# Kernel tuning notes

Hardware: AMD Instinct MI355X
Metric: run time of the kernel (lower is better)

## Reference

```python
import jax, jax.numpy as jnp
import numpy as np

D_MODEL = 1024
D_STATE = 16
D_CONV = 4
EXPAND = 2
D_INNER = D_MODEL * EXPAND
B_SZ, L_SEQ = 4, 1024


def setup_inputs() -> dict:
    key = jax.random.key(0)
    ks = jax.random.split(key, 8)
    s = lambda fan_in: 1.0 / np.sqrt(fan_in)
    x = jax.random.normal(ks[0], (B_SZ, L_SEQ, D_MODEL), dtype=jnp.float32)
    in_proj_w = jax.random.uniform(ks[1], (2 * D_INNER, D_MODEL), jnp.float32, -s(D_MODEL), s(D_MODEL))
    conv_w = jax.random.uniform(ks[2], (D_INNER, 1, D_CONV), jnp.float32, -s(D_CONV), s(D_CONV))
    conv_b = jax.random.uniform(ks[3], (D_INNER,), jnp.float32, -s(D_CONV), s(D_CONV))
    x_proj_w = jax.random.uniform(ks[4], (2 * D_STATE + D_INNER, D_INNER), jnp.float32, -s(D_INNER), s(D_INNER))
    dt_proj_w = jax.random.uniform(ks[5], (D_INNER, D_INNER), jnp.float32, -s(D_INNER), s(D_INNER))
    dt_proj_b = jax.random.uniform(ks[6], (D_INNER,), jnp.float32, -1e-3, 1e-3)
    A = jnp.tile(jnp.arange(1, D_STATE + 1, dtype=jnp.float32), (D_INNER, 1))
    A_log = jnp.log(A)
    D_param = jnp.ones((D_INNER,), jnp.float32)
    out_proj_w = jax.random.uniform(ks[7], (D_MODEL, D_INNER), jnp.float32, -s(D_INNER), s(D_INNER))
    return {"x": x, "in_proj_w": in_proj_w, "conv_w": conv_w, "conv_b": conv_b,
            "x_proj_w": x_proj_w, "dt_proj_w": dt_proj_w, "dt_proj_b": dt_proj_b,
            "A_log": A_log, "D_param": D_param, "out_proj_w": out_proj_w}


def _selective_scan(x, delta, Bp, Cp, A_log, D_param):
    # x, delta: [B, L, D]; Bp, Cp: [B, L, N]
    A = -jnp.exp(A_log)                                   # [D, N]
    deltaA = jnp.exp(delta[..., None] * A)                # [B, L, D, N]
    deltaB_x = delta[..., None] * Bp[:, :, None, :] * x[..., None]  # [B, L, D, N]

    def step(h, inp):
        dA, dBx, Ct = inp                                 # [B,D,N], [B,D,N], [B,N]
        h = dA * h + dBx
        y = jnp.einsum('bn,bdn->bd', Ct, h)
        return h, y

    h0 = jnp.zeros((x.shape[0], x.shape[2], A.shape[1]), x.dtype)
    xs = (jnp.swapaxes(deltaA, 0, 1), jnp.swapaxes(deltaB_x, 0, 1), jnp.swapaxes(Cp, 0, 1))
    _, ys = jax.lax.scan(step, h0, xs)                    # ys: [L, B, D]
    return jnp.swapaxes(ys, 0, 1) + x * D_param


def reference(x, in_proj_w, conv_w, conv_b, x_proj_w, dt_proj_w, dt_proj_b, A_log, D_param, out_proj_w):
    B, L, _ = x.shape
    xz = x @ in_proj_w.T                                  # [B, L, 2*D_inner]
    xi, z = jnp.split(xz, 2, axis=-1)
    # causal depthwise conv (pad left K-1 == pad both & truncate to L)
    xc = jnp.swapaxes(xi, 1, 2)                           # [B, D_inner, L]
    xc = jax.lax.conv_general_dilated(xc, conv_w, window_strides=(1,),
                                      padding=[(D_CONV - 1, 0)],
                                      feature_group_count=D_INNER,
                                      dimension_numbers=('NCH', 'OIH', 'NCH'))
    xc = xc + conv_b[None, :, None]
    xi = jax.nn.silu(jnp.swapaxes(xc, 1, 2))              # [B, L, D_inner]
    deltaBC = xi @ x_proj_w.T
    delta, Bp, Cp = jnp.split(deltaBC, [D_INNER, D_INNER + D_STATE], axis=-1)
    delta = jax.nn.softplus(delta @ dt_proj_w.T + dt_proj_b)
    y = _selective_scan(xi, delta, Bp, Cp, A_log, D_param)
    return (y * jax.nn.silu(z)) @ out_proj_w.T
```

## Files before the change

kernel.cpp:

```cpp
#include <hip/hip_runtime.h>
#include <math.h>

#define B_SZ 4
#define L_SEQ 1024
#define D_MODEL 1024
#define D_INNER 2048
#define D_STATE 16
#define N_BC 2080
#define M_ROWS (B_SZ * L_SEQ)
#define CHUNK 32
#define NCH (L_SEQ / CHUNK)

typedef unsigned short u16;
typedef __bf16 bf16x8 __attribute__((ext_vector_type(8)));
typedef float f32x4 __attribute__((ext_vector_type(4)));

typedef const __attribute__((address_space(1))) unsigned short glb_u16;
typedef __attribute__((address_space(3))) unsigned short lds_u16;

__device__ __forceinline__ void gload_lds16(const u16* g, u16* l) {
    __builtin_amdgcn_global_load_lds((glb_u16*)g, (lds_u16*)l, 16, 0, 0);
}

__device__ __forceinline__ float bf2f(u16 u) {
    union { unsigned int i; float f; } v; v.i = ((unsigned int)u) << 16; return v.f;
}
__device__ __forceinline__ u16 f2bf(float f) {
    union { float f; unsigned int i; } v; v.f = f;
    return (u16)((v.i + 0x7FFFu + ((v.i >> 16) & 1u)) >> 16);
}
__device__ __forceinline__ float softplus_f(float v) {
    return fmaxf(v, 0.f) + log1pf(expf(-fabsf(v)));
}
__device__ __forceinline__ float silu_f(float v) {
    return v / (1.f + expf(-v));
}

__global__ __launch_bounds__(256) void cvt5_bf16_k(
    const float* __restrict__ s0, const float* __restrict__ s1,
    const float* __restrict__ s2, const float* __restrict__ s3,
    const float* __restrict__ s4,
    u16* __restrict__ dst,
    int e0, int e1, int e2, int e3, int e4)
{
    int i = blockIdx.x * 256 + threadIdx.x;
    if (i >= e4) return;
    const float* src; int base;
    if (i < e0)      { src = s0; base = 0;  }
    else if (i < e1) { src = s1; base = e0; }
    else if (i < e2) { src = s2; base = e1; }
    else if (i < e3) { src = s3; base = e2; }
    else             { src = s4; base = e3; }
    float4 v = *(const float4*)(src + (size_t)(i - base) * 4);
    ushort4 o;
    o.x = f2bf(v.x); o.y = f2bf(v.y); o.z = f2bf(v.z); o.w = f2bf(v.w);
    *(ushort4*)(dst + (size_t)i * 4) = o;
}

__global__ __launch_bounds__(256) void transpose_cvt_k(
    const float* __restrict__ in,
    u16* __restrict__ outT)
{
    __shared__ float t[32][33];
    const int bx = blockIdx.x, by = blockIdx.y;
    const int r = threadIdx.x >> 5, c = threadIdx.x & 31;
#pragma unroll
    for (int i = 0; i < 4; ++i) {
        int kk = by * 32 + r + i * 8;
        int jj = bx * 32 + c;
        t[r + i * 8][c] = in[(size_t)kk * 2048 + jj];
    }
    __syncthreads();
#pragma unroll
    for (int i = 0; i < 4; ++i) {
        int jj = bx * 32 + r + i * 8;
        int kk = by * 32 + c;
        outT[(size_t)jj * 2048 + kk] = f2bf(t[c][r + i * 8]);
    }
}

template <int EPI, int BM, int BN, int WTM, int WTN>
__global__ __launch_bounds__((BM / WTM) * (BN / WTN) * 64, 2)
void gemm_bf16(
    const u16* __restrict__ A, int lda,
    const u16* __restrict__ W, int ldw,
    int M, int N, int K, int ldc,
    const float* __restrict__ bias,
    float* __restrict__ Cf, u16* __restrict__ Cb, float* __restrict__ Caux)
{
    constexpr int NWC = BN / WTN;
    constexpr int WAVES = (BM / WTM) * NWC;
    constexpr int MF = WTM / 16;
    constexpr int NF = WTN / 16;
    constexpr int CA = BM / 16;
    constexpr int CB = BN / 16;
    constexpr int CPW = (CA + CB) / WAVES;

    __shared__ __align__(16) u16 As[BM * 32];
    __shared__ __align__(16) u16 Ws[BN * 32];

    const unsigned nwg = gridDim.x * gridDim.y;
    const unsigned f = blockIdx.y * gridDim.x + blockIdx.x;
    const unsigned tile = (f & 7u) * (nwg >> 3) + (f >> 3);
    const int bxi = tile % gridDim.x;
    const int byi = tile / gridDim.x;

    const int tid = threadIdx.x;
    const int lane = tid & 63;
    const int wave = tid >> 6;
    const int wr = wave / NWC;
    const int wc = wave % NWC;
    const int bm = byi * BM;
    const int bn = bxi * BN;
    const int l15 = lane & 15;
    const int lq = lane >> 4;

    const int lrow = lane >> 2;
    const int qoff = (((lane & 3) ^ ((lane >> 3) & 3))) * 8;
    const int rq = ((lq ^ ((l15 >> 1) & 3))) * 8;

    f32x4 acc[MF][NF];
#pragma unroll
    for (int m = 0; m < MF; ++m)
#pragma unroll
        for (int n = 0; n < NF; ++n) acc[m][n] = f32x4{0.f, 0.f, 0.f, 0.f};

    const int nt = K >> 5;
    for (int t = 0; t < nt; ++t) {
        const int k0 = t << 5;
#pragma unroll
        for (int i = 0; i < CPW; ++i) {
            const int c = wave * CPW + i;
            if (c < CA) {
                const int row = c * 16 + lrow;
                gload_lds16(A + (size_t)(bm + row) * lda + k0 + qoff, &As[c * 512]);
            } else {
                const int cc = c - CA;
                const int row = cc * 16 + lrow;
                int wrow = bn + row; if (wrow >= N) wrow = N - 1;
                gload_lds16(W + (size_t)wrow * ldw + k0 + qoff, &Ws[cc * 512]);
            }
        }
        __syncthreads();

        bf16x8 af[MF], bfr[NF];
#pragma unroll
        for (int m = 0; m < MF; ++m) {
            int r = wr * WTM + m * 16 + l15;
            af[m] = *reinterpret_cast<const bf16x8*>(&As[r * 32 + rq]);
        }
#pragma unroll
        for (int n = 0; n < NF; ++n) {
            int r = wc * WTN + n * 16 + l15;
            bfr[n] = *reinterpret_cast<const bf16x8*>(&Ws[r * 32 + rq]);
        }
#pragma unroll
        for (int m = 0; m < MF; ++m)
#pragma unroll
            for (int n = 0; n < NF; ++n)
                acc[m][n] = __builtin_amdgcn_mfma_f32_16x16x32_bf16(af[m], bfr[n], acc[m][n], 0, 0, 0);

        __syncthreads();
    }

#pragma unroll
    for (int m = 0; m < MF; ++m) {
#pragma unroll
        for (int n = 0; n < NF; ++n) {
#pragma unroll
            for (int j = 0; j < 4; ++j) {
                int gr = bm + wr * WTM + m * 16 + lq * 4 + j;
                int gc = bn + wc * WTN + n * 16 + l15;
                float v = acc[m][n][j];
                if (EPI == 0) {
                    if (gc < N) Cf[(size_t)gr * ldc + gc] = v;
                } else if (EPI == 2) {
                    if (gc < N) Cb[(size_t)gr * ldc + gc] = f2bf(v);
                } else {
                    if (gc < D_INNER) Cf[(size_t)gr * D_INNER + gc] = softplus_f(v + bias[gc]);
                    else if (gc < N_BC) Caux[(size_t)gr * 32 + (gc - D_INNER)] = v;
                }
            }
        }
    }
}

__global__ __launch_bounds__(256) void conv_silu_k(
    const u16* __restrict__ xz,
    const float* __restrict__ cw,
    const float* __restrict__ cb,
    u16* __restrict__ xc)
{
    int idx = blockIdx.x * 256 + threadIdx.x;
    if (idx >= M_ROWS * D_INNER) return;
    int d = idx & (D_INNER - 1);
    int m = idx >> 11;
    int l = m & (L_SEQ - 1);
    float4 w = *(const float4*)(cw + d * 4);
    const u16* base = xz + (size_t)m * (2 * D_INNER) + d;
    float acc = cb[d];
    acc = fmaf(bf2f(base[0]), w.w, acc);
    if (l >= 1) acc = fmaf(bf2f(base[-(2 * D_INNER)]), w.z, acc);
    if (l >= 2) acc = fmaf(bf2f(base[-2 * (2 * D_INNER)]), w.y, acc);
    if (l >= 3) acc = fmaf(bf2f(base[-3 * (2 * D_INNER)]), w.x, acc);
    xc[idx] = f2bf(silu_f(acc));
}

__global__ __launch_bounds__(256) void scan_pass1(
    const float* __restrict__ delta,
    const u16* __restrict__ xc,
    const float* __restrict__ BC,
    const float* __restrict__ A_log,
    float* __restrict__ hbuf,
    float* __restrict__ sumd)
{
    __shared__ float Bs[CHUNK][16];
    const int bid = blockIdx.x;
    const int c = bid & (NCH - 1);
    const int dblk = (bid >> 5) & 7;
    const int b = bid >> 8;
    const int tid = threadIdx.x;
    const int d = dblk * 256 + tid;
    const int row0 = b * L_SEQ + c * CHUNK;

#pragma unroll
    for (int i = 0; i < 2; ++i) {
        int e = tid + i * 256;
        int l = e >> 4, n = e & 15;
        Bs[l][n] = BC[(size_t)(row0 + l) * 32 + n];
    }
    __syncthreads();

    float Ac[16], h[16];
#pragma unroll
    for (int n = 0; n < 16; ++n) { Ac[n] = -__expf(A_log[d * 16 + n]); h[n] = 0.f; }
    float sd = 0.f;

    for (int l = 0; l < CHUNK; ++l) {
        size_t r = (size_t)(row0 + l);
        float dv = delta[r * D_INNER + d];
        float xv = bf2f(xc[r * D_INNER + d]);
        float t = dv * xv;
        sd += dv;
#pragma unroll
        for (int n = 0; n < 16; ++n) {
            float dA = __expf(dv * Ac[n]);
            h[n] = fmaf(dA, h[n], t * Bs[l][n]);
        }
    }
    size_t base = ((size_t)(b * NCH + c) * 16) * D_INNER + d;
#pragma unroll
    for (int n = 0; n < 16; ++n) hbuf[base + (size_t)n * D_INNER] = h[n];
    sumd[(size_t)(b * NCH + c) * D_INNER + d] = sd;
}

__global__ __launch_bounds__(256) void scan_pass2(
    const float* __restrict__ A_log,
    const float* __restrict__ sumd,
    float* __restrict__ hbuf)
{
    const int bid = blockIdx.x;
    const int dblk = bid & 7;
    const int n = (bid >> 3) & 15;
    const int b = bid >> 7;
    const int d = dblk * 256 + threadIdx.x;
    const float Ac = -__expf(A_log[d * 16 + n]);
    float carry = 0.f;
    for (int c = 0; c < NCH; ++c) {
        float sd = sumd[(size_t)(b * NCH + c) * D_INNER + d];
        size_t idx = ((size_t)(b * NCH + c) * 16 + n) * D_INNER + d;
        float tmp = hbuf[idx];
        hbuf[idx] = carry;
        carry = fmaf(__expf(Ac * sd), carry, tmp);
    }
}

__global__ __launch_bounds__(256) void scan_pass3(
    const float* __restrict__ delta,
    const u16* __restrict__ xc,
    const float* __restrict__ BC,
    const u16* __restrict__ xz,
    const float* __restrict__ A_log,
    const float* __restrict__ Dp,
    const float* __restrict__ hbuf,
    u16* __restrict__ yg)
{
    __shared__ float BCs[CHUNK][32];
    const int bid = blockIdx.x;
    const int c = bid & (NCH - 1);
    const int dblk = (bid >> 5) & 7;
    const int b = bid >> 8;
    const int tid = threadIdx.x;
    const int d = dblk * 256 + tid;
    const int row0 = b * L_SEQ + c * CHUNK;

#pragma unroll
    for (int i = 0; i < (CHUNK * 32) / 256; ++i) {
        int e = tid + i * 256;
        int l = e >> 5, j = e & 31;
        BCs[l][j] = BC[(size_t)(row0 + l) * 32 + j];
    }
    __syncthreads();

    float Ac[16], h[16];
    size_t base = ((size_t)(b * NCH + c) * 16) * D_INNER + d;
#pragma unroll
    for (int n = 0; n < 16; ++n) {
        Ac[n] = -__expf(A_log[d * 16 + n]);
        h[n] = hbuf[base + (size_t)n * D_INNER];
    }
    const float Dv = Dp[d];

    for (int l = 0; l < CHUNK; ++l) {
        size_t r = (size_t)(row0 + l);
        float dv = delta[r * D_INNER + d];
        float xv = bf2f(xc[r * D_INNER + d]);
        float t = dv * xv;
        float y = xv * Dv;
#pragma unroll
        for (int n = 0; n < 16; ++n) {
            float dA = __expf(dv * Ac[n]);
            h[n] = fmaf(dA, h[n], t * BCs[l][n]);
            y = fmaf(BCs[l][16 + n], h[n], y);
        }
        float zv = bf2f(xz[r * (2 * D_INNER) + D_INNER + d]);
        yg[r * D_INNER + d] = f2bf(y * silu_f(zv));
    }
}

extern "C" void kernel_launch(void* const* d_in, const int* in_sizes, int n_in,
                              void* d_out, int out_size, void* d_ws, size_t ws_size,
                              hipStream_t stream)
{
    const float* x          = (const float*)d_in[0];
    const float* in_proj_w  = (const float*)d_in[1];
    const float* conv_w     = (const float*)d_in[2];
    const float* conv_b     = (const float*)d_in[3];
    const float* x_proj_w   = (const float*)d_in[4];
    const float* dt_proj_w  = (const float*)d_in[5];
    const float* dt_proj_b  = (const float*)d_in[6];
    const float* A_log      = (const float*)d_in[7];
    const float* D_param    = (const float*)d_in[8];
    const float* out_proj_w = (const float*)d_in[9];
    float* out = (float*)d_out;

    char* p = (char*)d_ws;
    u16* x_bf  = (u16*)p;  p += (size_t)M_ROWS * D_MODEL * 2;
    u16* w1_bf = (u16*)p;  p += (size_t)2 * D_INNER * D_MODEL * 2;
    u16* w3_bf = (u16*)p;  p += (size_t)N_BC * D_INNER * 2;
    u16* w4_bf = (u16*)p;  p += (size_t)D_INNER * D_INNER * 2;
    u16* w6_bf = (u16*)p;  p += (size_t)D_MODEL * D_INNER * 2;
    u16* xz_bf = (u16*)p;  p += (size_t)M_ROWS * 2 * D_INNER * 2;
    u16* xc_bf = (u16*)p;  p += (size_t)M_ROWS * D_INNER * 2;
    u16* dt_bf = (u16*)p;  p += (size_t)M_ROWS * D_INNER * 2;
    float* BC  = (float*)p; p += (size_t)M_ROWS * 32 * 4;
    float* delta = (float*)p; p += (size_t)M_ROWS * D_INNER * 4;
    u16* yg_bf = (u16*)p;
    u16* wxT = dt_bf;
    float* hbuf = (float*)dt_bf;
    float* sumd = (float*)x_bf;

    dim3 blk(256);

    {
        const int n0 = (M_ROWS * D_MODEL) / 4;
        const int n1 = (2 * D_INNER * D_MODEL) / 4;
        const int n2 = (N_BC * D_INNER) / 4;
        const int n3 = (D_INNER * D_INNER) / 4;
        const int n4 = (D_MODEL * D_INNER) / 4;
        const int e0 = n0, e1 = e0 + n1, e2 = e1 + n2, e3 = e2 + n3, e4 = e3 + n4;
        cvt5_bf16_k<<<dim3((e4 + 255) / 256), blk, 0, stream>>>(
            x, in_proj_w, x_proj_w, dt_proj_w, out_proj_w,
            x_bf, e0, e1, e2, e3, e4);
    }

    gemm_bf16<2, 128, 128, 64, 64><<<dim3(32, 32), blk, 0, stream>>>(
        x_bf, D_MODEL, w1_bf, D_MODEL, M_ROWS, 2 * D_INNER, D_MODEL, 2 * D_INNER,
        nullptr, nullptr, xz_bf, nullptr);

    conv_silu_k<<<dim3((M_ROWS * D_INNER) / 256), blk, 0, stream>>>(
        xz_bf, conv_w, conv_b, xc_bf);

    transpose_cvt_k<<<dim3(64, 64), blk, 0, stream>>>(x_proj_w, wxT);

    gemm_bf16<2, 128, 128, 64, 64><<<dim3(16, 16), blk, 0, stream>>>(
        w4_bf, D_INNER, wxT, D_INNER, D_INNER, D_INNER, D_INNER, D_INNER,
        nullptr, nullptr, w3_bf, nullptr);

    gemm_bf16<5, 128, 128, 64, 64><<<dim3(17, 32), blk, 0, stream>>>(
        xc_bf, D_INNER, w3_bf, D_INNER, M_ROWS, N_BC, D_INNER, 0,
        dt_proj_b, delta, nullptr, BC);

    scan_pass1<<<dim3(B_SZ * 8 * NCH), blk, 0, stream>>>(
        delta, xc_bf, BC, A_log, hbuf, sumd);
    scan_pass2<<<dim3(B_SZ * 16 * 8), blk, 0, stream>>>(
        A_log, sumd, hbuf);
    scan_pass3<<<dim3(B_SZ * 8 * NCH), blk, 0, stream>>>(
        delta, xc_bf, BC, xz_bf, A_log, D_param, hbuf, yg_bf);

    gemm_bf16<0, 128, 128, 64, 64><<<dim3(8, 32), blk, 0, stream>>>(
        yg_bf, D_INNER, w6_bf, D_INNER, M_ROWS, D_MODEL, D_INNER, D_MODEL,
        nullptr, out, nullptr, nullptr);
}
```

Measured before the change: 359.8 us.

## Double GEMM K-step to 64 with new LDS swizzle, vectorize conv

The bf16 GEMM now stages a K=64 slice per iteration (two MFMA sub-steps per barrier pair), halving the number of __syncthreads and load rounds, with a new 8-way XOR swizzle for the 64-wide LDS rows. The grouped workgroup-to-tile remapping is removed, so tiles map directly from blockIdx, which may hurt L2 locality. The conv+SiLU kernel processes four channels per thread with vectorized ushort4 loads and stores. LDS use doubles per block, which could affect occupancy.

Result: faster. 350.6 us (-2.6%).

```diff
diff --git a/kernel.cpp b/kernel.cpp
--- a/kernel.cpp
+++ b/kernel.cpp
@@ -92,32 +92,29 @@
     constexpr int WAVES = (BM / WTM) * NWC;
     constexpr int MF = WTM / 16;
     constexpr int NF = WTN / 16;
-    constexpr int CA = BM / 16;
-    constexpr int CB = BN / 16;
-    constexpr int CPW = (CA + CB) / WAVES;
-
-    __shared__ __align__(16) u16 As[BM * 32];
-    __shared__ __align__(16) u16 Ws[BN * 32];
-
-    const unsigned nwg = gridDim.x * gridDim.y;
-    const unsigned f = blockIdx.y * gridDim.x + blockIdx.x;
-    const unsigned tile = (f & 7u) * (nwg >> 3) + (f >> 3);
-    const int bxi = tile % gridDim.x;
-    const int byi = tile / gridDim.x;
+    constexpr int CAK = BM / 8;
+    constexpr int CBK = BN / 8;
+    constexpr int APW = CAK / WAVES;
+    constexpr int BPW = CBK / WAVES;
+
+    __shared__ __align__(16) u16 As[BM * 64];
+    __shared__ __align__(16) u16 Ws[BN * 64];
 
     const int tid = threadIdx.x;
     const int lane = tid & 63;
     const int wave = tid >> 6;
     const int wr = wave / NWC;
     const int wc = wave % NWC;
-    const int bm = byi * BM;
-    const int bn = bxi * BN;
+    const int bm = blockIdx.y * BM;
+    const int bn = blockIdx.x * BN;
     const int l15 = lane & 15;
     const int lq = lane >> 4;
 
-    const int lrow = lane >> 2;
-    const int qoff = (((lane & 3) ^ ((lane >> 3) & 3))) * 8;
-    const int rq = ((lq ^ ((l15 >> 1) & 3))) * 8;
+    const int srow = lane >> 3;
+    const int sq = ((lane & 7) ^ srow) * 8;
+    const int x7 = l15 & 7;
+    const int rq0 = ((0 + lq) ^ x7) * 8;
+    const int rq1 = ((4 + lq) ^ x7) * 8;
 
     f32x4 acc[MF][NF];
 #pragma unroll
@@ -125,40 +122,44 @@
 #pragma unroll
         for (int n = 0; n < NF; ++n) acc[m][n] = f32x4{0.f, 0.f, 0.f, 0.f};
 
-    const int nt = K >> 5;
+    const int nt = K >> 6;
     for (int t = 0; t < nt; ++t) {
-        const int k0 = t << 5;
-#pragma unroll
-        for (int i = 0; i < CPW; ++i) {
-            const int c = wave * CPW + i;
-            if (c < CA) {
-                const int row = c * 16 + lrow;
-                gload_lds16(A + (size_t)(bm + row) * lda + k0 + qoff, &As[c * 512]);
-            } else {
-                const int cc = c - CA;
-                const int row = cc * 16 + lrow;
-                int wrow = bn + row; if (wrow >= N) wrow = N - 1;
-                gload_lds16(W + (size_t)wrow * ldw + k0 + qoff, &Ws[cc * 512]);
+        const int k0 = t << 6;
+#pragma unroll
+        for (int i = 0; i < APW; ++i) {
+            const int c = wave * APW + i;
+            const int row = c * 8 + srow;
+            gload_lds16(A + (size_t)(bm + row) * lda + k0 + sq, &As[c * 512]);
+        }
+#pragma unroll
+        for (int i = 0; i < BPW; ++i) {
+            const int c = wave * BPW + i;
+            const int row = c * 8 + srow;
+            int wrow = bn + row; if (wrow >= N) wrow = N - 1;
+            gload_lds16(W + (size_t)wrow * ldw + k0 + sq, &Ws[c * 512]);
+        }
+        __syncthreads();
+
+#pragma unroll
+        for (int s = 0; s < 2; ++s) {
+            const int rq = s ? rq1 : rq0;
+            bf16x8 af[MF], bfr[NF];
+#pragma unroll
+            for (int m = 0; m < MF; ++m) {
+                int r = wr * WTM + m * 16 + l15;
+                af[m] = *reinterpret_cast<const bf16x8*>(&As[r * 64 + rq]);
             }
-        }
-        __syncthreads();
-
-        bf16x8 af[MF], bfr[NF];
-#pragma unroll
-        for (int m = 0; m < MF; ++m) {
-            int r = wr * WTM + m * 16 + l15;
-            af[m] = *reinterpret_cast<const bf16x8*>(&As[r * 32 + rq]);
-        }
-#pragma unroll
-        for (int n = 0; n < NF; ++n) {
-            int r = wc * WTN + n * 16 + l15;
-            bfr[n] = *reinterpret_cast<const bf16x8*>(&Ws[r * 32 + rq]);
-        }
-#pragma unroll
-        for (int m = 0; m < MF; ++m)
-#pragma unroll
-            for (int n = 0; n < NF; ++n)
-                acc[m][n] = __builtin_amdgcn_mfma_f32_16x16x32_bf16(af[m], bfr[n], acc[m][n], 0, 0, 0);
+#pragma unroll
+            for (int n = 0; n < NF; ++n) {
+                int r = wc * WTN + n * 16 + l15;
+                bfr[n] = *reinterpret_cast<const bf16x8*>(&Ws[r * 64 + rq]);
+            }
+#pragma unroll
+            for (int m = 0; m < MF; ++m)
+#pragma unroll
+                for (int n = 0; n < NF; ++n)
+                    acc[m][n] = __builtin_amdgcn_mfma_f32_16x16x32_bf16(af[m], bfr[n], acc[m][n], 0, 0, 0);
+        }
 
         __syncthreads();
     }
@@ -192,18 +193,32 @@
     u16* __restrict__ xc)
 {
     int idx = blockIdx.x * 256 + threadIdx.x;
-    if (idx >= M_ROWS * D_INNER) return;
-    int d = idx & (D_INNER - 1);
-    int m = idx >> 11;
+    if (idx >= M_ROWS * (D_INNER / 4)) return;
+    int d4 = idx & (D_INNER / 4 - 1);
+    int m = idx >> 9;
     int l = m & (L_SEQ - 1);
-    float4 w = *(const float4*)(cw + d * 4);
+    int d = d4 * 4;
     const u16* base = xz + (size_t)m * (2 * D_INNER) + d;
-    float acc = cb[d];
-    acc = fmaf(bf2f(base[0]), w.w, acc);
-    if (l >= 1) acc = fmaf(bf2f(base[-(2 * D_INNER)]), w.z, acc);
-    if (l >= 2) acc = fmaf(bf2f(base[-2 * (2 * D_INNER)]), w.y, acc);
-    if (l >= 3) acc = fmaf(bf2f(base[-3 * (2 * D_INNER)]), w.x, acc);
-    xc[idx] = f2bf(silu_f(acc));
+    float4 w0 = *(const float4*)(cw + (d + 0) * 4);
+    float4 w1 = *(const float4*)(cw + (d + 1) * 4);
+    float4 w2 = *(const float4*)(cw + (d + 2) * 4);
+    float4 w3 = *(const float4*)(cw + (d + 3) * 4);
+    float4 b4 = *(const float4*)(cb + d);
+    float a0 = b4.x, a1 = b4.y, a2 = b4.z, a3 = b4.w;
+#pragma unroll
+    for (int t = 0; t < 4; ++t) {
+        if (l >= t) {
+            ushort4 v = *(const ushort4*)(base - (size_t)t * (2 * D_INNER));
+            a0 = fmaf(bf2f(v.x), (&w0.x)[3 - t], a0);
+            a1 = fmaf(bf2f(v.y), (&w1.x)[3 - t], a1);
+            a2 = fmaf(bf2f(v.z), (&w2.x)[3 - t], a2);
+            a3 = fmaf(bf2f(v.w), (&w3.x)[3 - t], a3);
+        }
+    }
+    ushort4 o;
+    o.x = f2bf(silu_f(a0)); o.y = f2bf(silu_f(a1));
+    o.z = f2bf(silu_f(a2)); o.w = f2bf(silu_f(a3));
+    *(ushort4*)(xc + (size_t)m * D_INNER + d) = o;
 }
 
 __global__ __launch_bounds__(256) void scan_pass1(
@@ -378,7 +393,7 @@
         x_bf, D_MODEL, w1_bf, D_MODEL, M_ROWS, 2 * D_INNER, D_MODEL, 2 * D_INNER,
         nullptr, nullptr, xz_bf, nullptr);
 
-    conv_silu_k<<<dim3((M_ROWS * D_INNER) / 256), blk, 0, stream>>>(
+    conv_silu_k<<<dim3((M_ROWS * (D_INNER / 4)) / 256), blk, 0, stream>>>(
         xz_bf, conv_w, conv_b, xc_bf);
 
     transpose_cvt_k<<<dim3(64, 64), blk, 0, stream>>>(x_proj_w, wxT);
```
